# Kernel tuning notes

Measured on AMD Instinct MI355X. Metric: run time of the kernel, lower is better.

Reference implementation:

```python
import jax, jax.numpy as jnp
import numpy as np

C = 512
GROUPS = 32
EPS = 1e-6

def setup_inputs() -> dict:
    key = jax.random.key(0)
    ks = jax.random.split(key, 6)
    s = 1.0 / np.sqrt(C)
    return {
        "x": jax.random.normal(ks[0], (2, C, 16, 32, 32), dtype=jnp.float32),
        "gamma": jnp.ones((C,), jnp.float32),
        "beta": jnp.zeros((C,), jnp.float32),
        "q_w": jax.random.normal(ks[1], (C, C), jnp.float32) * s,
        "q_b": jnp.zeros((C,), jnp.float32),
        "k_w": jax.random.normal(ks[2], (C, C), jnp.float32) * s,
        "k_b": jnp.zeros((C,), jnp.float32),
        "v_w": jax.random.normal(ks[3], (C, C), jnp.float32) * s,
        "v_b": jnp.zeros((C,), jnp.float32),
        "proj_w": jax.random.normal(ks[4], (C, C), jnp.float32) * s,
        "proj_b": jnp.zeros((C,), jnp.float32),
    }

def _group_norm(x, gamma, beta):
    # x: [b, c, t, h, w]
    b, c, t, h, w = x.shape
    xg = x.reshape(b, GROUPS, c // GROUPS, t, h, w)
    mean = xg.mean(axis=(2, 3, 4, 5), keepdims=True)
    var = xg.var(axis=(2, 3, 4, 5), keepdims=True)
    xg = (xg - mean) * jax.lax.rsqrt(var + EPS)
    x = xg.reshape(b, c, t, h, w)
    return x * gamma[None, :, None, None, None] + beta[None, :, None, None, None]

def _pw_conv(x, w, bias):
    # 1x1x1 conv == channel GEMM. x: [b,c,t,h,w], w: [c_out, c_in]
    y = jnp.einsum('bcthw,oc->bothw', x, w)
    return y + bias[None, :, None, None, None]

def reference(x, gamma, beta, q_w, q_b, k_w, k_b, v_w, v_b, proj_w, proj_b):
    b, c, t, h, w = x.shape
    hn = _group_norm(x, gamma, beta)
    q = _pw_conv(hn, q_w, q_b)
    k = _pw_conv(hn, k_w, k_b)
    v = _pw_conv(hn, v_w, v_b)
    # [b,c,t,h,w] -> [b*t, h*w, c]
    def to_seq(a):
        return jnp.transpose(a, (0, 2, 3, 4, 1)).reshape(b * t, h * w, c)
    q, k, v = to_seq(q), to_seq(k), to_seq(v)
    scale = 1.0 / jnp.sqrt(jnp.asarray(c, x.dtype))
    attn = jnp.einsum('bqc,bkc->bqk', q, k) * scale  # [b*t, hw, hw]
    attn = jax.nn.softmax(attn, axis=-1)
    out = jnp.einsum('bqk,bkc->bqc', attn, v)
    out = out.reshape(b, t, h, w, c).transpose(0, 4, 1, 2, 3)
    return x + _pw_conv(out, proj_w, proj_b)
```

## Files before the change

kernel.cpp:

```cpp
#include <hip/hip_runtime.h>

typedef unsigned short u16;
typedef __attribute__((ext_vector_type(8))) short bf16x8;
typedef __attribute__((ext_vector_type(4))) float f32x4;

#define DEV static __device__ __forceinline__

DEV u16 f2bf(float f) {
  union { float f; unsigned u; } x; x.f = f;
  return (u16)((x.u + 0x7FFFu + ((x.u >> 16) & 1u)) >> 16);
}
DEV float bf2f(u16 h) { union { unsigned u; float f; } x; x.u = ((unsigned)h) << 16; return x.f; }

DEV void gload16(const void* g, void* l) {
  __builtin_amdgcn_global_load_lds((const __attribute__((address_space(1))) void*)g,
                                   (__attribute__((address_space(3))) void*)l, 16, 0, 0);
}

DEV int eswz(int r) { return (((r & 7) ^ ((r >> 3) & 7)) << 4); }

#define SM_SCALE 0.044194173824159216f

__global__ __launch_bounds__(256) void gn_stats_a(const float* __restrict__ x,
                                                  float2* __restrict__ part) {
  const int bg = blockIdx.x >> 5, slice = blockIdx.x & 31;
  const float* base = x + (long)bg * 262144 + slice * 8192;
  float s = 0.f, q = 0.f;
#pragma unroll
  for (int i = 0; i < 8; ++i) {
    float4 v = *(const float4*)(base + i * 1024 + threadIdx.x * 4);
    s += v.x + v.y + v.z + v.w;
    q += v.x * v.x + v.y * v.y + v.z * v.z + v.w * v.w;
  }
#pragma unroll
  for (int o = 32; o; o >>= 1) { s += __shfl_xor(s, o); q += __shfl_xor(q, o); }
  __shared__ float2 red[4];
  if ((threadIdx.x & 63) == 0) red[threadIdx.x >> 6] = make_float2(s, q);
  __syncthreads();
  if (threadIdx.x == 0) {
    float S = 0.f, Q = 0.f;
    for (int i = 0; i < 4; ++i) { S += red[i].x; Q += red[i].y; }
    part[blockIdx.x] = make_float2(S, Q);
  }
}

__global__ void gn_stats_b(const float2* __restrict__ part, float2* __restrict__ stats) {
  float s = 0.f, q = 0.f;
  if (threadIdx.x < 32) {
    float2 p = part[blockIdx.x * 32 + threadIdx.x];
    s = p.x; q = p.y;
  }
#pragma unroll
  for (int o = 32; o; o >>= 1) { s += __shfl_xor(s, o); q += __shfl_xor(q, o); }
  if (threadIdx.x == 0) {
    const float inv = 1.f / 262144.f;
    float mean = s * inv;
    float var = q * inv - mean * mean;
    stats[blockIdx.x] = make_float2(mean, rsqrtf(var + 1e-6f));
  }
}

__global__ __launch_bounds__(256) void gn_apply(const float* __restrict__ x,
                                                const float* __restrict__ gamma,
                                                const float* __restrict__ beta,
                                                const float2* __restrict__ stats,
                                                u16* __restrict__ hn) {
  __shared__ u16 tile[64][65];
  const int p0 = blockIdx.x * 64, c0 = blockIdx.y * 64, bt = blockIdx.z;
  const int b = bt >> 4, t = bt & 15, tid = threadIdx.x;
  const float* xb = x + (long)b * 8388608 + t * 1024;
#pragma unroll 4
  for (int r = 0; r < 16; ++r) {
    int ci = r * 4 + (tid >> 6), pi = tid & 63;
    int c = c0 + ci;
    float2 st = stats[b * 32 + (c >> 4)];
    float v = xb[(long)c * 16384 + p0 + pi];
    v = (v - st.x) * st.y * gamma[c] + beta[c];
    tile[ci][pi] = f2bf(v);
  }
  __syncthreads();
  u16* hb = hn + ((long)bt * 1024 + p0) * 512 + c0;
#pragma unroll 4
  for (int r = 0; r < 16; ++r) {
    int pi = r * 4 + (tid >> 6), ci = tid & 63;
    hb[(long)pi * 512 + ci] = tile[ci][pi];
  }
}

__global__ __launch_bounds__(256) void prep(const float* __restrict__ w0, const float* __restrict__ w1,
                                            const float* __restrict__ w2, const float* __restrict__ w3,
                                            const float* __restrict__ qb, const float* __restrict__ kb,
                                            const float* __restrict__ vb,
                                            u16* __restrict__ dst, float* __restrict__ bias) {
  if (blockIdx.x < 1024) {
    int e = (blockIdx.x * 256 + threadIdx.x) * 4;
    const float* src = w0;
    int which = e >> 18, off = e & 262143;
    if (which == 1) src = w1; else if (which == 2) src = w2; else if (which == 3) src = w3;
    float4 v = *(const float4*)(src + off);
    ushort4 o;
    o.x = f2bf(v.x); o.y = f2bf(v.y); o.z = f2bf(v.z); o.w = f2bf(v.w);
    *(ushort4*)(dst + e) = o;
  } else {
    for (int i = threadIdx.x; i < 1536; i += 256) {
      float v = (i < 512) ? qb[i] : (i < 1024) ? kb[i - 512] : vb[i - 1024];
      bias[i] = v;
    }
  }
}

__global__ __launch_bounds__(256) void softmax_rows_bf16(u16* __restrict__ scores) {
  const int wave = threadIdx.x >> 6, lane = threadIdx.x & 63;
  const long row = (long)blockIdx.x * 4 + wave;
  u16* srow = scores + row * 1024;
  bf16x8 a0 = *(const bf16x8*)(srow + lane * 16);
  bf16x8 a1 = *(const bf16x8*)(srow + lane * 16 + 8);
  float v[16];
#pragma unroll
  for (int j = 0; j < 8; ++j) { v[j] = bf2f((u16)a0[j]); v[8 + j] = bf2f((u16)a1[j]); }
  float m = v[0];
#pragma unroll
  for (int j = 1; j < 16; ++j) m = fmaxf(m, v[j]);
#pragma unroll
  for (int o = 32; o; o >>= 1) m = fmaxf(m, __shfl_xor(m, o));
  float s = 0.f, e[16];
#pragma unroll
  for (int j = 0; j < 16; ++j) { e[j] = __expf((v[j] - m) * SM_SCALE); s += e[j]; }
#pragma unroll
  for (int o = 32; o; o >>= 1) s += __shfl_xor(s, o);
  const float inv = 1.f / s;
  bf16x8 o0, o1;
#pragma unroll
  for (int j = 0; j < 8; ++j) {
    o0[j] = (short)f2bf(e[j] * inv);
    o1[j] = (short)f2bf(e[8 + j] * inv);
  }
  *(bf16x8*)(srow + lane * 16) = o0;
  *(bf16x8*)(srow + lane * 16 + 8) = o1;
}

__global__ __launch_bounds__(256) void sm_stats(const u16* __restrict__ scores,
                                                float2* __restrict__ rowstats) {
  const int wave = threadIdx.x >> 6, lane = threadIdx.x & 63;
  const long row = (long)blockIdx.x * 4 + wave;
  const u16* srow = scores + row * 1024;
  bf16x8 a0 = *(const bf16x8*)(srow + lane * 16);
  bf16x8 a1 = *(const bf16x8*)(srow + lane * 16 + 8);
  float v[16];
#pragma unroll
  for (int j = 0; j < 8; ++j) {
    v[j] = bf2f((u16)a0[j]) * SM_SCALE;
    v[8 + j] = bf2f((u16)a1[j]) * SM_SCALE;
  }
  float m = v[0];
#pragma unroll
  for (int j = 1; j < 16; ++j) m = fmaxf(m, v[j]);
#pragma unroll
  for (int o = 32; o; o >>= 1) m = fmaxf(m, __shfl_xor(m, o));
  float s = 0.f;
#pragma unroll
  for (int j = 0; j < 16; ++j) s += __expf(v[j] - m);
#pragma unroll
  for (int o = 32; o; o >>= 1) s += __shfl_xor(s, o);
  if (lane == 0) rowstats[row] = make_float2(m, 1.f / s);
}

template <int EPI, int ASRC>
__global__ __launch_bounds__(512, 4) void gemmk(
    const u16* __restrict__ A, int lda, long sA,
    const u16* __restrict__ B, int ldb, long sB,
    u16* __restrict__ Cv, int ldc, long sC,
    const float* __restrict__ bias, int K,
    const float* __restrict__ xin, float* __restrict__ outp,
    u16* __restrict__ vT, const float2* __restrict__ rowstats) {
  __shared__ u16 sm[3 * 12288];
  char* smc = (char*)sm;
  const int tid = threadIdx.x, wid = tid >> 6, lane = tid & 63;
  const int wm = wid >> 2, wn = wid & 3;

  int bx = blockIdx.x, by = blockIdx.y, bz = blockIdx.z;
  {
    unsigned gx = gridDim.x, gy = gridDim.y;
    unsigned total = gx * gy * gridDim.z;
    if ((total & 7u) == 0) {
      unsigned gxy = gx * gy;
      unsigned d = (blockIdx.z * gy + blockIdx.y) * gx + blockIdx.x;
      unsigned w = (d & 7u) * (total >> 3) + (d >> 3);
      bz = w / gxy; unsigned r = w - (unsigned)bz * gxy;
      bx = r / gy;  by = r - (unsigned)bx * gy;
    }
  }
  const long m0 = (long)bx * 128, n0 = (long)by * 256;
  const char* Bb = (const char*)(B + (long)bz * sB + n0 * ldb);
  const int NT = K >> 5;
  const long lda2 = 2L * lda, ldb2 = 2L * ldb;

  const int srow = tid >> 2;
  const int cb = ((tid & 3) * 16) ^ (((srow >> 1) & 3) << 4);
  const int dA = srow * 64 + (tid & 3) * 16;
  const int dAsw = srow * 64 + cb;
  const int dB0 = 8192 + dA, dB1 = 16384 + dA;
  const char* gB0 = Bb + (long)srow * ldb2 + cb;
  const char* gB1 = Bb + (long)(srow + 128) * ldb2 + cb;

  const int lrow = lane & 15, kslot = (lane >> 4) * 16;
  const int fsw = ((lrow >> 1) & 3) << 4;
  const int aoff = (wm * 64 + lrow) * 64 + (kslot ^ fsw);
  const int boff = 8192 + (wn * 64 + lrow) * 64 + (kslot ^ fsw);

  f32x4 acc[4][4] = {};

  if (ASRC == 0) {
    const char* gA = (const char*)(A + (long)bz * sA + m0 * lda) + (long)srow * lda2 + cb;
#define STG3(off) do { gload16(gA, smc + (off) + dA); \
                       gload16(gB0, smc + (off) + dB0); \
                       gload16(gB1, smc + (off) + dB1); } while (0)
    STG3(0);
    gA += 64; gB0 += 64; gB1 += 64;
    if (NT > 1) { STG3(24576); gA += 64; gB0 += 64; gB1 += 64; }
    if (NT > 1) asm volatile("s_waitcnt vmcnt(3)" ::: "memory");
    else        asm volatile("s_waitcnt vmcnt(0)" ::: "memory");
    __builtin_amdgcn_s_barrier();

    int cb_cur = 0, cb_stg = 49152;
    for (int T = 0; T < NT; ++T) {
      const bool s2 = (T + 2 < NT);
      if (s2) { STG3(cb_stg); gA += 64; gB0 += 64; gB1 += 64; }
      const char* ba = smc + cb_cur;
      bf16x8 af[4], bf[4];
#pragma unroll
      for (int mi = 0; mi < 4; ++mi) af[mi] = *(const bf16x8*)(ba + aoff + mi * 1024);
#pragma unroll
      for (int ni = 0; ni < 4; ++ni) bf[ni] = *(const bf16x8*)(ba + boff + ni * 1024);
      __builtin_amdgcn_s_setprio(1);
#pragma unroll
      for (int mi = 0; mi < 4; ++mi)
#pragma unroll
        for (int ni = 0; ni < 4; ++ni)
          acc[mi][ni] = __builtin_amdgcn_mfma_f32_16x16x32_bf16(af[mi], bf[ni], acc[mi][ni], 0, 0, 0);
      __builtin_amdgcn_s_setprio(0);
      if (s2) asm volatile("s_waitcnt vmcnt(3)" ::: "memory");
      else    asm volatile("s_waitcnt vmcnt(0)" ::: "memory");
      __builtin_amdgcn_s_barrier();
      cb_cur = (cb_cur == 49152) ? 0 : cb_cur + 24576;
      cb_stg = (cb_stg == 49152) ? 0 : cb_stg + 24576;
    }
#undef STG3
  } else {
    const float2 rs = rowstats[(long)bz * 1024 + m0 + srow];
    const float mneg = -rs.x, invS = rs.y;
    const u16* gAr = A + (long)bz * sA + (m0 + srow) * (long)lda + (tid & 3) * 8;
    bf16x8 aCur;
#define STGB(off) do { gload16(gB0, smc + (off) + dB0); \
                       gload16(gB1, smc + (off) + dB1); } while (0)
#define XFORM(dstoff) do { u16 tmp_[8]; \
      _Pragma("unroll") \
      for (int j_ = 0; j_ < 8; ++j_) { \
        float f_ = bf2f((u16)aCur[j_]); \
        tmp_[j_] = f2bf(__expf(fmaf(f_, SM_SCALE, mneg)) * invS); \
      } \
      *(bf16x8*)(smc + (dstoff) + dAsw) = *(bf16x8*)tmp_; } while (0)

    aCur = *(const bf16x8*)gAr;
    STGB(0);
    gB0 += 64; gB1 += 64;
    if (NT > 1) { STGB(24576); gB0 += 64; gB1 += 64; }
    if (NT > 1) asm volatile("s_waitcnt vmcnt(2)" ::: "memory");
    else        asm volatile("s_waitcnt vmcnt(0)" ::: "memory");
    XFORM(0);
    asm volatile("s_waitcnt lgkmcnt(0)" ::: "memory");
    __builtin_amdgcn_s_barrier();

    int cb_cur = 0, cb_nxt = 24576, cb_stg = 49152;
    for (int T = 0; T < NT; ++T) {
      const bool s1 = (T + 1 < NT), s2 = (T + 2 < NT);
      bf16x8 aNext;
      if (s1) aNext = *(const bf16x8*)(gAr + (T + 1) * 32);
      if (s2) { STGB(cb_stg); gB0 += 64; gB1 += 64; }
      const char* ba = smc + cb_cur;
      bf16x8 af[4], bf[4];
#pragma unroll
      for (int mi = 0; mi < 4; ++mi) af[mi] = *(const bf16x8*)(ba + aoff + mi * 1024);
#pragma unroll
      for (int ni = 0; ni < 4; ++ni) bf[ni] = *(const bf16x8*)(ba + boff + ni * 1024);
      __builtin_amdgcn_s_setprio(1);
#pragma unroll
      for (int mi = 0; mi < 4; ++mi)
#pragma unroll
        for (int ni = 0; ni < 4; ++ni)
          acc[mi][ni] = __builtin_amdgcn_mfma_f32_16x16x32_bf16(af[mi], bf[ni], acc[mi][ni], 0, 0, 0);
      __builtin_amdgcn_s_setprio(0);
      if (s2)      asm volatile("s_waitcnt vmcnt(2)" ::: "memory");
      else         asm volatile("s_waitcnt vmcnt(0)" ::: "memory");
      if (s1) { aCur = aNext; XFORM(cb_nxt); }
      asm volatile("s_waitcnt lgkmcnt(0)" ::: "memory");
      __builtin_amdgcn_s_barrier();
      cb_cur = cb_nxt;
      cb_nxt = cb_stg;
      cb_stg = (cb_stg == 49152) ? 0 : cb_stg + 24576;
    }
#undef STGB
#undef XFORM
  }

  __syncthreads();
  {
    const int lc = lane & 15, lr = (lane >> 4) * 4;
    char* wb_ = smc + wid * 8192;
#pragma unroll
    for (int ni = 0; ni < 4; ++ni) {
      float bv = 0.f;
      if (EPI == 1) bv = bias[n0 + wn * 64 + ni * 16 + lc];
#pragma unroll
      for (int mi = 0; mi < 4; ++mi)
#pragma unroll
        for (int j = 0; j < 4; ++j) {
          int rml = mi * 16 + lr + j;
          int colb = (ni * 32 + lc * 2) ^ eswz(rml);
          *(u16*)(wb_ + rml * 128 + colb) = f2bf(acc[mi][ni][j] + bv);
        }
    }
  }
  __syncthreads();

  if (EPI == 2) {
    const int bt = (int)(m0 >> 10), p0i = (int)(m0 & 1023);
    const int b = bt >> 4, t = bt & 15;
    const int p8 = (tid & 15) * 8, cl = tid >> 4;
#pragma unroll
    for (int ci = 0; ci < 8; ++ci) {
      int c = ci * 32 + cl;
      const long base = (long)b * 8388608 + (long)(n0 + c) * 16384 + t * 1024 + p0i + p8;
      const float bv = bias[n0 + c];
      const int reg = (((p8 >> 6) << 2) | (c >> 6)) * 8192;
      const int c2 = (c & 63) * 2;
      float vals[8];
#pragma unroll
      for (int j = 0; j < 8; ++j) {
        int r = (p8 + j) & 63;
        vals[j] = bf2f(*(const u16*)(smc + reg + r * 128 + (c2 ^ eswz(r))));
      }
      float4 x0 = *(const float4*)(xin + base);
      float4 x1 = *(const float4*)(xin + base + 4);
      float4 o0 = make_float4(x0.x + bv + vals[0], x0.y + bv + vals[1],
                              x0.z + bv + vals[2], x0.w + bv + vals[3]);
      float4 o1 = make_float4(x1.x + bv + vals[4], x1.y + bv + vals[5],
                              x1.z + bv + vals[6], x1.w + bv + vals[7]);
      *(float4*)(outp + base) = o0;
      *(float4*)(outp + base + 4) = o1;
    }
  } else if (EPI == 1 && n0 >= 1024) {
    const int bt = (int)(m0 >> 10), p0i = (int)(m0 & 1023);
    const int p8 = (tid & 15) * 8, cl = tid >> 4;
    u16* vbase = vT + (long)bt * 524288 + (long)(n0 - 1024) * 1024 + p0i;
#pragma unroll
    for (int ci = 0; ci < 8; ++ci) {
      int c = ci * 32 + cl;
      const int reg = (((p8 >> 6) << 2) | (c >> 6)) * 8192;
      const int c2 = (c & 63) * 2;
      u16 tmp[8];
#pragma unroll
      for (int j = 0; j < 8; ++j) {
        int r = (p8 + j) & 63;
        tmp[j] = *(const u16*)(smc + reg + r * 128 + (c2 ^ eswz(r)));
      }
      *(bf16x8*)(vbase + (long)c * 1024 + p8) = *(bf16x8*)tmp;
    }
  } else {
    u16* C = Cv + (long)bz * sC;
    const int c8 = tid & 31, r0e = tid >> 5;
#pragma unroll
    for (int i = 0; i < 8; ++i) {
      int r = r0e + i * 16;
      int rwid = ((r >> 6) << 2) | (c8 >> 3);
      int rr = r & 63;
      bf16x8 v = *(const bf16x8*)(smc + rwid * 8192 + rr * 128 +
                                  (((c8 & 7) * 16) ^ eswz(rr)));
      *(bf16x8*)(C + (m0 + r) * (long)ldc + n0 + c8 * 8) = v;
    }
  }
}

extern "C" void kernel_launch(void* const* d_in, const int* in_sizes, int n_in,
                              void* d_out, int out_size, void* d_ws, size_t ws_size,
                              hipStream_t stream) {
  (void)in_sizes; (void)n_in; (void)out_size;
  const float* x      = (const float*)d_in[0];
  const float* gamma  = (const float*)d_in[1];
  const float* beta   = (const float*)d_in[2];
  const float* q_w    = (const float*)d_in[3];
  const float* q_b    = (const float*)d_in[4];
  const float* k_w    = (const float*)d_in[5];
  const float* k_b    = (const float*)d_in[6];
  const float* v_w    = (const float*)d_in[7];
  const float* v_b    = (const float*)d_in[8];
  const float* proj_w = (const float*)d_in[9];
  const float* proj_b = (const float*)d_in[10];

  const size_t OFF_WB    = 0;
  const size_t OFF_BIAS  = 2097152;
  const size_t OFF_STATS = 2103296;
  const size_t OFF_PART  = 2103808;
  const size_t OFF_HN    = 2121728;
  const size_t OFF_QK    = 35676160;
  const size_t OFF_VT    = 102785024;
  const size_t OFF_SC    = 136339456;
  const size_t OFF_RS    = 203448320;

  char* ws = (char*)d_ws;
  u16*    wb      = (u16*)(ws + OFF_WB);
  float*  qkvbias = (float*)(ws + OFF_BIAS);
  float2* stats   = (float2*)(ws + OFF_STATS);
  float2* part    = (float2*)(ws + OFF_PART);
  u16*    hn      = (u16*)(ws + OFF_HN);
  u16*    ob      = hn;
  u16*    qk      = (u16*)(ws + OFF_QK);
  u16*    vT      = (u16*)(ws + OFF_VT);
  u16*    scores  = (u16*)(ws + OFF_SC);
  float2* rowstats = (float2*)(ws + OFF_RS);

  const bool FUSED = (ws_size >= OFF_RS + 262144);
  const int CH = FUSED ? 32 : 8;

  prep<<<1025, 256, 0, stream>>>(q_w, k_w, v_w, proj_w, q_b, k_b, v_b, wb, qkvbias);
  gn_stats_a<<<2048, 256, 0, stream>>>(x, part);
  gn_stats_b<<<64, 64, 0, stream>>>(part, stats);
  gn_apply<<<dim3(16, 8, 32), 256, 0, stream>>>(x, gamma, beta, stats, hn);

  gemmk<1, 0><<<dim3(256, 6, 1), 512, 0, stream>>>(
      hn, 512, 0, wb, 512, 0, qk, 1024, 0, qkvbias, 512, nullptr, nullptr, vT, nullptr);

  for (int ch = 0; ch < 32 / CH; ++ch) {
    long f0 = (long)ch * CH;
    gemmk<0, 0><<<dim3(8, 4, CH), 512, 0, stream>>>(
        qk + f0 * 1048576, 1024, 1048576,
        qk + 512 + f0 * 1048576, 1024, 1048576,
        scores, 1024, 1048576, nullptr, 512, nullptr, nullptr, nullptr, nullptr);
    if (FUSED) {
      sm_stats<<<CH * 256, 256, 0, stream>>>(scores, rowstats);
      gemmk<0, 1><<<dim3(8, 2, CH), 512, 0, stream>>>(
          scores, 1024, 1048576,
          vT + f0 * 524288, 1024, 524288,
          ob + f0 * 524288, 512, 524288, nullptr, 1024, nullptr, nullptr, nullptr, rowstats);
    } else {
      softmax_rows_bf16<<<CH * 256, 256, 0, stream>>>(scores);
      gemmk<0, 0><<<dim3(8, 2, CH), 512, 0, stream>>>(
          scores, 1024, 1048576,
          vT + f0 * 524288, 1024, 524288,
          ob + f0 * 524288, 512, 524288, nullptr, 1024, nullptr, nullptr, nullptr, nullptr);
    }
  }

  gemmk<2, 0><<<dim3(256, 2, 1), 512, 0, stream>>>(
      ob, 512, 0, wb + 786432, 512, 0, nullptr, 0, 0, proj_b, 512,
      x, (float*)d_out, nullptr, nullptr);
}
```

Baseline: 261.0 us.

## Fuse softmax row statistics into PV GEMM and drop sm_stats pass

Removes the separate sm_stats kernel that read all bf16 scores to compute the row max and inverse sum. The PV GEMM now computes exp(score*scale) without subtracting the max, accumulates the row sum while transforming A tiles, and scales the output accumulators by 1/sum in the epilogue through a small shared array. This saves a full read pass over the score matrix and a kernel launch per chunk. The risk is numerical: without max subtraction, exp can overflow for large scores, and the unnormalized bf16 probabilities lose relative precision.

Result: no change. 256.0 us (median of 3 runs) (-1.9%).

```diff
diff --git a/kernel.cpp b/kernel.cpp
--- a/kernel.cpp
+++ b/kernel.cpp
@@ -139,32 +139,6 @@
   *(bf16x8*)(srow + lane * 16 + 8) = o1;
 }
 
-__global__ __launch_bounds__(256) void sm_stats(const u16* __restrict__ scores,
-                                                float2* __restrict__ rowstats) {
-  const int wave = threadIdx.x >> 6, lane = threadIdx.x & 63;
-  const long row = (long)blockIdx.x * 4 + wave;
-  const u16* srow = scores + row * 1024;
-  bf16x8 a0 = *(const bf16x8*)(srow + lane * 16);
-  bf16x8 a1 = *(const bf16x8*)(srow + lane * 16 + 8);
-  float v[16];
-#pragma unroll
-  for (int j = 0; j < 8; ++j) {
-    v[j] = bf2f((u16)a0[j]) * SM_SCALE;
-    v[8 + j] = bf2f((u16)a1[j]) * SM_SCALE;
-  }
-  float m = v[0];
-#pragma unroll
-  for (int j = 1; j < 16; ++j) m = fmaxf(m, v[j]);
-#pragma unroll
-  for (int o = 32; o; o >>= 1) m = fmaxf(m, __shfl_xor(m, o));
-  float s = 0.f;
-#pragma unroll
-  for (int j = 0; j < 16; ++j) s += __expf(v[j] - m);
-#pragma unroll
-  for (int o = 32; o; o >>= 1) s += __shfl_xor(s, o);
-  if (lane == 0) rowstats[row] = make_float2(m, 1.f / s);
-}
-
 template <int EPI, int ASRC>
 __global__ __launch_bounds__(512, 4) void gemmk(
     const u16* __restrict__ A, int lda, long sA,
@@ -172,8 +146,9 @@
     u16* __restrict__ Cv, int ldc, long sC,
     const float* __restrict__ bias, int K,
     const float* __restrict__ xin, float* __restrict__ outp,
-    u16* __restrict__ vT, const float2* __restrict__ rowstats) {
+    u16* __restrict__ vT) {
   __shared__ u16 sm[3 * 12288];
+  __shared__ float rsuminv[128];
   char* smc = (char*)sm;
   const int tid = threadIdx.x, wid = tid >> 6, lane = tid & 63;
   const int wm = wid >> 2, wn = wid & 3;
@@ -247,17 +222,17 @@
     }
 #undef STG3
   } else {
-    const float2 rs = rowstats[(long)bz * 1024 + m0 + srow];
-    const float mneg = -rs.x, invS = rs.y;
     const u16* gAr = A + (long)bz * sA + (m0 + srow) * (long)lda + (tid & 3) * 8;
     bf16x8 aCur;
+    float psum = 0.f;
 #define STGB(off) do { gload16(gB0, smc + (off) + dB0); \
                        gload16(gB1, smc + (off) + dB1); } while (0)
 #define XFORM(dstoff) do { u16 tmp_[8]; \
       _Pragma("unroll") \
       for (int j_ = 0; j_ < 8; ++j_) { \
-        float f_ = bf2f((u16)aCur[j_]); \
-        tmp_[j_] = f2bf(__expf(fmaf(f_, SM_SCALE, mneg)) * invS); \
+        float e_ = __expf(bf2f((u16)aCur[j_]) * SM_SCALE); \
+        psum += e_; \
+        tmp_[j_] = f2bf(e_); \
       } \
       *(bf16x8*)(smc + (dstoff) + dAsw) = *(bf16x8*)tmp_; } while (0)
 
@@ -301,6 +276,9 @@
     }
 #undef STGB
 #undef XFORM
+    psum += __shfl_xor(psum, 1);
+    psum += __shfl_xor(psum, 2);
+    if ((tid & 3) == 0) rsuminv[srow] = 1.f / psum;
   }
 
   __syncthreads();
@@ -317,7 +295,9 @@
         for (int j = 0; j < 4; ++j) {
           int rml = mi * 16 + lr + j;
           int colb = (ni * 32 + lc * 2) ^ eswz(rml);
-          *(u16*)(wb_ + rml * 128 + colb) = f2bf(acc[mi][ni][j] + bv);
+          float v = acc[mi][ni][j];
+          if (ASRC == 1) v *= rsuminv[wm * 64 + rml];
+          *(u16*)(wb_ + rml * 128 + colb) = f2bf(v + bv);
         }
     }
   }
@@ -405,7 +385,6 @@
   const size_t OFF_QK    = 35676160;
   const size_t OFF_VT    = 102785024;
   const size_t OFF_SC    = 136339456;
-  const size_t OFF_RS    = 203448320;
 
   char* ws = (char*)d_ws;
   u16*    wb      = (u16*)(ws + OFF_WB);
@@ -417,9 +396,8 @@
   u16*    qk      = (u16*)(ws + OFF_QK);
   u16*    vT      = (u16*)(ws + OFF_VT);
   u16*    scores  = (u16*)(ws + OFF_SC);
-  float2* rowstats = (float2*)(ws + OFF_RS);
-
-  const bool FUSED = (ws_size >= OFF_RS + 262144);
+
+  const bool FUSED = (ws_size >= OFF_SC + 32ULL * 2097152);
   const int CH = FUSED ? 32 : 8;
 
   prep<<<1025, 256, 0, stream>>>(q_w, k_w, v_w, proj_w, q_b, k_b, v_b, wb, qkvbias);
@@ -428,30 +406,29 @@
   gn_apply<<<dim3(16, 8, 32), 256, 0, stream>>>(x, gamma, beta, stats, hn);
 
   gemmk<1, 0><<<dim3(256, 6, 1), 512, 0, stream>>>(
-      hn, 512, 0, wb, 512, 0, qk, 1024, 0, qkvbias, 512, nullptr, nullptr, vT, nullptr);
+      hn, 512, 0, wb, 512, 0, qk, 1024, 0, qkvbias, 512, nullptr, nullptr, vT);
 
   for (int ch = 0; ch < 32 / CH; ++ch) {
     long f0 = (long)ch * CH;
     gemmk<0, 0><<<dim3(8, 4, CH), 512, 0, stream>>>(
         qk + f0 * 1048576, 1024, 1048576,
         qk + 512 + f0 * 1048576, 1024, 1048576,
-        scores, 1024, 1048576, nullptr, 512, nullptr, nullptr, nullptr, nullptr);
+        scores, 1024, 1048576, nullptr, 512, nullptr, nullptr, nullptr);
     if (FUSED) {
-      sm_stats<<<CH * 256, 256, 0, stream>>>(scores, rowstats);
       gemmk<0, 1><<<dim3(8, 2, CH), 512, 0, stream>>>(
           scores, 1024, 1048576,
           vT + f0 * 524288, 1024, 524288,
-          ob + f0 * 524288, 512, 524288, nullptr, 1024, nullptr, nullptr, nullptr, rowstats);
+          ob + f0 * 524288, 512, 524288, nullptr, 1024, nullptr, nullptr, nullptr);
     } else {
       softmax_rows_bf16<<<CH * 256, 256, 0, stream>>>(scores);
       gemmk<0, 0><<<dim3(8, 2, CH), 512, 0, stream>>>(
           scores, 1024, 1048576,
           vT + f0 * 524288, 1024, 524288,
-          ob + f0 * 524288, 512, 524288, nullptr, 1024, nullptr, nullptr, nullptr, nullptr);
+          ob + f0 * 524288, 512, 524288, nullptr, 1024, nullptr, nullptr, nullptr);
     }
   }
 
   gemmk<2, 0><<<dim3(256, 2, 1), 512, 0, stream>>>(
       ob, 512, 0, wb + 786432, 512, 0, nullptr, 0, 0, proj_b, 512,
-      x, (float*)d_out, nullptr, nullptr);
-}
+      x, (float*)d_out, nullptr);
+}
```
